# Optimization experiments

Hardware: AMD Instinct MI355X
Metric: run time of the kernel (lower is better)

## Reference

```python
import jax, jax.numpy as jnp
import numpy as np
import math

ANCHOR_SIZES = (128.0, 256.0, 512.0)
ANCHOR_RATIOS = (0.5, 1.0, 2.0)
NMS_THRESH = 0.7
PRE_NMS_TOPK = 6000   # rpn_test_prenms_topk (module is in eval at __init__)
POST_NMS_TOPK = 300   # rpn_test_topk
MIN_SIZE = 16.0
BBOX_CLIP = math.log(1000.0 / 16.0)


def _base_anchors():
    scales = jnp.array(ANCHOR_SIZES, jnp.float32)
    ratios = jnp.array(ANCHOR_RATIOS, jnp.float32)
    h_r = jnp.sqrt(ratios)
    w_r = 1.0 / h_r
    ws = (w_r[:, None] * scales[None, :]).reshape(-1)  # [A], ratio-major
    hs = (h_r[:, None] * scales[None, :]).reshape(-1)
    return jnp.stack([-ws, -hs, ws, hs], axis=1) * 0.5  # [A,4] centered at origin


def _grid_anchors(img_hw, feat_hw):
    Hi, Wi = img_hw
    Hf, Wf = feat_hw
    sy, sx = Hi // Hf, Wi // Wf  # feature stride
    shift_x = jnp.arange(Wf, dtype=jnp.float32) * sx
    shift_y = jnp.arange(Hf, dtype=jnp.float32) * sy
    yy, xx = jnp.meshgrid(shift_y, shift_x, indexing='ij')
    shifts = jnp.stack([xx, yy, xx, yy], axis=-1).reshape(-1, 1, 4)
    # layout (H, W, A) matches permute(0,2,3,1) flattening of the heads
    return (shifts + _base_anchors()[None]).reshape(-1, 4)


def _conv(x, w, b, pad):
    y = jax.lax.conv_general_dilated(x, w, (1, 1), pad,
                                     dimension_numbers=('NCHW', 'OIHW', 'NCHW'))
    return y + b[None, :, None, None]


def _decode(deltas, anchors):
    wa = anchors[:, 2] - anchors[:, 0]
    ha = anchors[:, 3] - anchors[:, 1]
    cxa = anchors[:, 0] + 0.5 * wa
    cya = anchors[:, 1] + 0.5 * ha
    dx, dy = deltas[:, 0], deltas[:, 1]
    dw = jnp.minimum(deltas[:, 2], BBOX_CLIP)
    dh = jnp.minimum(deltas[:, 3], BBOX_CLIP)
    cx = dx * wa + cxa
    cy = dy * ha + cya
    w = jnp.exp(dw) * wa
    h = jnp.exp(dh) * ha
    return jnp.stack([cx - 0.5 * w, cy - 0.5 * h, cx + 0.5 * w, cy + 0.5 * h], axis=1)


def _pairwise_iou(a, b):
    area_a = (a[:, 2] - a[:, 0]) * (a[:, 3] - a[:, 1])
    area_b = (b[:, 2] - b[:, 0]) * (b[:, 3] - b[:, 1])
    lt = jnp.maximum(a[:, None, :2], b[None, :, :2])
    rb = jnp.minimum(a[:, None, 2:], b[None, :, 2:])
    wh = jnp.clip(rb - lt, 0.0)
    inter = wh[..., 0] * wh[..., 1]
    return inter / (area_a[:, None] + area_b[None, :] - inter)


def _nms_keep(boxes, valid, thresh):
    # boxes are already sorted by descending score; greedy suppression
    N = boxes.shape[0]
    iou = _pairwise_iou(boxes, boxes)  # [N,N]
    idx = jnp.arange(N)

    def body(i, keep):
        sup = keep[i] & (iou[i] > thresh) & (idx > i)
        return keep & jnp.logical_not(sup)

    return jax.lax.fori_loop(0, N, body, valid)


def setup_inputs() -> dict:
    key = jax.random.key(0)
    ks = jax.random.split(key, 6)
    C, Hf, Wf = 1024, 100, 100
    Hi, Wi = 1600, 1600
    A = len(ANCHOR_SIZES) * len(ANCHOR_RATIOS)  # 9
    std = 0.01  # matches torch.nn.init.normal_(std=0.01), bias=0
    return {
        'input_image': jax.random.normal(ks[0], (1, 3, Hi, Wi), jnp.float32),
        'feature_map': jax.random.normal(ks[1], (1, C, Hf, Wf), jnp.float32),
        'conv_w': jax.random.normal(ks[2], (C, C, 3, 3), jnp.float32) * std,
        'conv_b': jnp.zeros((C,), jnp.float32),
        'obj_w': jax.random.normal(ks[3], (A, C, 1, 1), jnp.float32) * std,
        'obj_b': jnp.zeros((A,), jnp.float32),
        'reg_w': jax.random.normal(ks[4], (4 * A, C, 1, 1), jnp.float32) * std,
        'reg_b': jnp.zeros((4 * A,), jnp.float32),
    }


def reference(input_image, feature_map, conv_w, conv_b, obj_w, obj_b, reg_w, reg_b):
    Hi, Wi = input_image.shape[-2:]
    Hf, Wf = feature_map.shape[-2:]
    A = obj_w.shape[0]

    feats = jax.nn.relu(_conv(feature_map, conv_w, conv_b, 'SAME'))
    obj = _conv(feats, obj_w, obj_b, 'VALID')   # [N,A,Hf,Wf]
    reg = _conv(feats, reg_w, reg_b, 'VALID')   # [N,4A,Hf,Wf]

    obj_flat = jnp.transpose(obj, (0, 2, 3, 1)).reshape(-1)                 # [N*Hf*Wf*A]
    reg_flat = jnp.transpose(reg.reshape(-1, A, 4, Hf, Wf),
                             (0, 3, 4, 1, 2)).reshape(-1, 4)                # [N*Hf*Wf*A,4]

    anchors = _grid_anchors((Hi, Wi), (Hf, Wf))
    boxes = _decode(jax.lax.stop_gradient(reg_flat), anchors)
    probs = jax.nn.sigmoid(jax.lax.stop_gradient(obj_flat))

    k = min(PRE_NMS_TOPK, probs.shape[0])
    top_p, top_i = jax.lax.top_k(probs, k)
    b = boxes[top_i]
    b = jnp.stack([jnp.clip(b[:, 0], 0.0, Wi), jnp.clip(b[:, 1], 0.0, Hi),
                   jnp.clip(b[:, 2], 0.0, Wi), jnp.clip(b[:, 3], 0.0, Hi)], axis=1)
    valid = ((b[:, 2] - b[:, 0]) >= MIN_SIZE) & ((b[:, 3] - b[:, 1]) >= MIN_SIZE)

    keep = _nms_keep(b, valid, NMS_THRESH)
    masked = jnp.where(keep, top_p, -1.0)
    final_s, fi = jax.lax.top_k(masked, POST_NMS_TOPK)
    final_b = b[fi]
    good = final_s > 0.0  # zero-pad slots beyond the NMS survivor count
    proposals = jnp.where(good[:, None], final_b, 0.0)
    scores = jnp.where(good, final_s, 0.0)
    return proposals, scores
```

## Files before the change

kernel.cpp:

```cpp
#include <hip/hip_runtime.h>
#include <stdint.h>

typedef unsigned int uint32;
typedef unsigned long long uint64;

#define NPIX      10000
#define NCH       1024
#define NANCH     90000
#define PRE_TOPK  6000
#define POST_TOPK 300
#define SORT_N    8192
#define NWORDS    94
#define SUP_ROWS  6016
#define BBOX_CLIP_F 4.135166556742356f

#define TILE_H   8
#define TILE_W   16
#define HALO_H   10
#define HALO_W   18
#define HALO_WP  20
#define CICHUNK  16
#define C_PER_WAVE 16

__device__ __forceinline__ uint64 shfl64(uint64 v, int lane) {
    int lo = __shfl((int)(uint32)v, lane);
    int hi = __shfl((int)(uint32)(v >> 32), lane);
    return ((uint64)(uint32)hi << 32) | (uint32)lo;
}

__global__ __launch_bounds__(256) void zero_out(float* __restrict__ out, int n) {
    int i = blockIdx.x * 256 + threadIdx.x;
    if (i < n) out[i] = 0.f;
}

__global__ __launch_bounds__(256) void repack_w3(const float* __restrict__ w, float* __restrict__ W3) {
    int cot = blockIdx.x;
    int cib = blockIdx.y;
    int t = threadIdx.x;
    int c = t & 15;
    int cil = t >> 4;
    int ci = (cib << 6) | (cil << 2);
    int co = (cot << 4) | c;
#pragma unroll
    for (int r = 0; r < 4; ++r) {
        const float* src = w + ((size_t)co * 1024 + (ci + r)) * 9;
        float* dst = W3 + (((size_t)cot * 1024 + (ci + r)) * 9) * 16 + c;
#pragma unroll
        for (int kk = 0; kk < 9; ++kk)
            dst[kk * 16] = src[kk];
    }
}

__global__ __launch_bounds__(256) void conv_sw2(const float* __restrict__ fm,
        const float* __restrict__ W3, const float* __restrict__ bias,
        float* __restrict__ feats) {
    __shared__ float xt[CICHUNK][HALO_H][HALO_WP];
    const int t = threadIdx.x;
    const int lane = t & 63;
    const int wv = t >> 6;
    const int tile = blockIdx.x;
    const int tx0 = (tile % 7) * TILE_W;
    const int ty0 = (tile / 7) * TILE_H;
    const int cot = __builtin_amdgcn_readfirstlane((blockIdx.y << 2) + wv);
    const int co0 = cot << 4;
    const int ly = lane >> 3, lx = lane & 7;

    float acc0[C_PER_WAVE] = {};
    float acc1[C_PER_WAVE] = {};

#pragma unroll 1
    for (int c0 = 0; c0 < NCH; c0 += CICHUNK) {
        __syncthreads();
        for (int i = t; i < CICHUNK * HALO_H * HALO_W; i += 256) {
            int ci = i / (HALO_H * HALO_W);
            int rem = i - ci * (HALO_H * HALO_W);
            int hy = rem / HALO_W;
            int hx = rem - hy * HALO_W;
            int gy = ty0 - 1 + hy;
            int gx = tx0 - 1 + hx;
            bool ok = (gy >= 0) & (gy < 100) & (gx >= 0) & (gx < 100);
            xt[ci][hy][hx] = ok ? fm[(size_t)(c0 + ci) * NPIX + gy * 100 + gx] : 0.f;
        }
        __syncthreads();
#pragma unroll 1
        for (int ci = 0; ci < CICHUNK; ++ci) {
            const float* wb = W3 + (((size_t)cot * 1024 + (size_t)(c0 + ci)) * 9) * 16;
#pragma unroll
            for (int kk = 0; kk < 9; ++kk) {
                const int ky = kk / 3, kx2 = kk % 3;
                float x0v = xt[ci][ly + ky][lx + kx2];
                float x1v = xt[ci][ly + ky][lx + 8 + kx2];
#pragma unroll
                for (int c = 0; c < C_PER_WAVE; ++c) {
                    float wgt = wb[kk * 16 + c];
                    acc0[c] = fmaf(wgt, x0v, acc0[c]);
                    acc1[c] = fmaf(wgt, x1v, acc1[c]);
                }
            }
        }
    }

    const int gy = ty0 + ly;
    const int gx0 = tx0 + lx;
    const int gx1 = tx0 + 8 + lx;
    const bool oky = gy < 100;
#pragma unroll
    for (int c = 0; c < C_PER_WAVE; ++c) {
        float b = bias[co0 + c];
        if (oky && (gx0 < 100)) feats[(size_t)(co0 + c) * NPIX + gy * 100 + gx0] = fmaxf(acc0[c] + b, 0.f);
        if (oky && (gx1 < 100)) feats[(size_t)(co0 + c) * NPIX + gy * 100 + gx1] = fmaxf(acc1[c] + b, 0.f);
    }
}

__global__ __launch_bounds__(256) void heads(const float* __restrict__ feats,
        const float* __restrict__ objw, const float* __restrict__ objb,
        const float* __restrict__ regw, const float* __restrict__ regb,
        uint32* __restrict__ keys32, float* __restrict__ regflat) {
    int p0 = blockIdx.x << 6;
    int t = threadIdx.x;
    int pl = t & 63;
    int g = t >> 6;
    __shared__ float fts[64][65];
    __shared__ float wl[48][64];
    float acc[12] = {};
    for (int c0 = 0; c0 < 1024; c0 += 64) {
        __syncthreads();
#pragma unroll
        for (int r = 0; r < 16; ++r) {
            int cc = g + (r << 2);
            int p = p0 + pl;
            fts[cc][pl] = (p < NPIX) ? feats[(size_t)(c0 + cc) * NPIX + p] : 0.f;
        }
#pragma unroll
        for (int i = 0; i < 12; ++i) {
            int flat = (i << 8) + t;
            int o = flat >> 6;
            int cc = flat & 63;
            float v = 0.f;
            if (o < 9) v = objw[o * 1024 + c0 + cc];
            else if (o < 45) v = regw[(o - 9) * 1024 + c0 + cc];
            wl[o][cc] = v;
        }
        __syncthreads();
#pragma unroll 16
        for (int cc = 0; cc < 64; ++cc) {
            float v = fts[cc][pl];
#pragma unroll
            for (int i = 0; i < 12; ++i)
                acc[i] = fmaf(v, wl[g + (i << 2)][cc], acc[i]);
        }
    }
    int p = p0 + pl;
    if (p < NPIX) {
#pragma unroll
        for (int i = 0; i < 12; ++i) {
            int o = g + (i << 2);
            if (o < 9) {
                float logit = acc[i] + objb[o];
                float prob = 1.f / (1.f + expf(-logit));
                keys32[p * 9 + o] = 0xFFFFFFFFu - __float_as_uint(prob);
            } else if (o < 45) {
                int ch = o - 9;
                float v = acc[i] + regb[ch];
                int a = ch >> 2, d = ch & 3;
                regflat[((size_t)p * 9 + a) * 4 + d] = v;
            }
        }
    }
}

__global__ __launch_bounds__(1024) void radix_select(const uint32* __restrict__ keys, uint32* __restrict__ meta) {
    __shared__ uint32 hist[256];
    __shared__ uint32 sPrefix, sK;
    int t = threadIdx.x;
    if (t == 0) { sPrefix = 0; sK = PRE_TOPK; }
    for (int pass = 0; pass < 4; ++pass) {
        int shift = 24 - pass * 8;
        uint32 kmask = pass ? (0xFFFFFFFFu << (32 - 8 * pass)) : 0u;
        if (t < 256) hist[t] = 0;
        __syncthreads();
        uint32 pref = sPrefix;
        for (int i = t; i < NANCH; i += 1024) {
            uint32 k = keys[i];
            if ((k & kmask) == pref) atomicAdd(&hist[(k >> shift) & 255], 1u);
        }
        __syncthreads();
        if (t == 0) {
            uint32 cum = 0, K = sK;
            for (int b = 0; b < 256; ++b) {
                uint32 c = hist[b];
                if (cum + c >= K) { sPrefix = pref | ((uint32)b << shift); sK = K - cum; break; }
                cum += c;
            }
        }
        __syncthreads();
    }
    if (t == 0) meta[0] = sPrefix;
}

__global__ __launch_bounds__(256) void compact_k(const uint32* __restrict__ keys, const uint32* __restrict__ meta,
        uint32* __restrict__ cnt, uint64* __restrict__ sel) {
    int i = blockIdx.x * 256 + threadIdx.x;
    if (i >= NANCH) return;
    uint32 T = meta[0];
    uint32 k = keys[i];
    if (k <= T) {
        uint32 pos = atomicAdd(cnt, 1u);
        if (pos < SORT_N) sel[pos] = ((uint64)k << 32) | (uint32)i;
    }
}

__global__ __launch_bounds__(1024) void bitonic_sort(const uint32* __restrict__ meta, const uint64* __restrict__ sel,
        uint64* __restrict__ sorted) {
    __shared__ uint64 arr[SORT_N];
    int t = threadIdx.x;
    uint32 cnt = meta[1]; if (cnt > SORT_N) cnt = SORT_N;
    for (int i = t; i < SORT_N; i += 1024) arr[i] = (i < (int)cnt) ? sel[i] : 0xFFFFFFFFFFFFFFFFull;
    __syncthreads();
    for (unsigned k = 2; k <= SORT_N; k <<= 1) {
        for (unsigned j = k >> 1; j > 0; j >>= 1) {
#pragma unroll 1
            for (int s = 0; s < SORT_N / 1024; ++s) {
                unsigned i = s * 1024 + t;
                unsigned l = i ^ j;
                if (l > i) {
                    uint64 a = arr[i], b = arr[l];
                    bool up = ((i & k) == 0);
                    if ((a > b) == up) { arr[i] = b; arr[l] = a; }
                }
            }
            __syncthreads();
        }
    }
    for (int i = t; i < PRE_TOPK; i += 1024) sorted[i] = arr[i];
}

__global__ __launch_bounds__(256) void decode_k(const uint64* __restrict__ sorted,
        const float* __restrict__ regflat,
        float4* __restrict__ boxes, float* __restrict__ probv, uint32* __restrict__ valid) {
    int i = blockIdx.x * 256 + threadIdx.x;
    if (i >= PRE_TOPK) return;
    uint64 v = sorted[i];
    uint32 idx = (uint32)v;
    uint32 key = (uint32)(v >> 32);
    float prob = __uint_as_float(0xFFFFFFFFu - key);
    int a = idx % 9;
    int p = idx / 9;
    int y = p / 100;
    int x = p - y * 100;
    const float ratios[3] = {0.5f, 1.0f, 2.0f};
    const float scales[3] = {128.f, 256.f, 512.f};
    float ratio = ratios[a / 3];
    float scale = scales[a % 3];
    float h_r = sqrtf(ratio);
    float w_r = 1.0f / h_r;
    float wsz = w_r * scale;
    float hsz = h_r * scale;
    float sx = 16.f * (float)x;
    float sy = 16.f * (float)y;
    float ax1 = sx - wsz * 0.5f;
    float ay1 = sy - hsz * 0.5f;
    float ax2 = sx + wsz * 0.5f;
    float ay2 = sy + hsz * 0.5f;
    float wa = ax2 - ax1;
    float ha = ay2 - ay1;
    float cxa = ax1 + 0.5f * wa;
    float cya = ay1 + 0.5f * ha;
    float dx = regflat[(size_t)idx * 4 + 0];
    float dy = regflat[(size_t)idx * 4 + 1];
    float dw = fminf(regflat[(size_t)idx * 4 + 2], BBOX_CLIP_F);
    float dh = fminf(regflat[(size_t)idx * 4 + 3], BBOX_CLIP_F);
    float cx = dx * wa + cxa;
    float cy = dy * ha + cya;
    float w = expf(dw) * wa;
    float h = expf(dh) * ha;
    float x1 = cx - 0.5f * w, y1 = cy - 0.5f * h, x2 = cx + 0.5f * w, y2 = cy + 0.5f * h;
    x1 = fminf(fmaxf(x1, 0.f), 1600.f);
    y1 = fminf(fmaxf(y1, 0.f), 1600.f);
    x2 = fminf(fmaxf(x2, 0.f), 1600.f);
    y2 = fminf(fmaxf(y2, 0.f), 1600.f);
    boxes[i] = make_float4(x1, y1, x2, y2);
    probv[i] = prob;
    valid[i] = (((x2 - x1) >= 16.f) & ((y2 - y1) >= 16.f)) ? 1u : 0u;
}

__global__ __launch_bounds__(64) void nms_pairs(const float4* __restrict__ boxes, uint64* __restrict__ sup) {
    int bi = blockIdx.y, bj = blockIdx.x;
    int t = threadIdx.x;
    int i = bi * 64 + t;
    if (bj < bi) { if (i < SUP_ROWS) sup[(size_t)i * NWORDS + bj] = 0; return; }
    __shared__ float4 bx[64];
    __shared__ float ab[64];
    int j0 = bj * 64;
    float4 bb = (j0 + t < PRE_TOPK) ? boxes[j0 + t] : make_float4(0, 0, 0, 0);
    bx[t] = bb;
    ab[t] = (bb.z - bb.x) * (bb.w - bb.y);
    __syncthreads();
    uint64 bits = 0;
    if (i < PRE_TOPK) {
        float4 ba = boxes[i];
        float aa = (ba.z - ba.x) * (ba.w - ba.y);
        for (int jj = 0; jj < 64; ++jj) {
            int j = j0 + jj;
            if (j > i && j < PRE_TOPK) {
                float4 bv = bx[jj];
                float ltx = fmaxf(ba.x, bv.x);
                float lty = fmaxf(ba.y, bv.y);
                float rbx = fminf(ba.z, bv.z);
                float rby = fminf(ba.w, bv.w);
                float wv = fmaxf(rbx - ltx, 0.f);
                float hv = fmaxf(rby - lty, 0.f);
                float inter = wv * hv;
                float iou = inter / (aa + ab[jj] - inter);
                if (iou > 0.7f) bits |= (1ull << jj);
            }
        }
    }
    if (i < SUP_ROWS) sup[(size_t)i * NWORDS + bj] = bits;
}

__global__ __launch_bounds__(64) void nms_scan(const uint32* __restrict__ valid, const uint64* __restrict__ sup,
        uint32* __restrict__ keeplist, uint32* __restrict__ kcount) {
    int l = threadIdx.x;
    __shared__ uint64 srow[64][95];
    uint64 r0 = 0, r1 = 0;
    for (int b = 0; b < 64; ++b) {
        int idx = l * 64 + b;
        if (idx < PRE_TOPK && valid[idx]) r0 |= (1ull << b);
    }
    if (l < NWORDS - 64) {
        int base = (64 + l) * 64;
        for (int b = 0; b < 64; ++b) {
            int idx = base + b;
            if (idx < PRE_TOPK && valid[idx]) r1 |= (1ull << b);
        }
    }
    int outc = 0;
    bool done = false;
    for (int c = 0; c < NWORDS && !done; ++c) {
        __syncthreads();
        for (int rr = 0; rr < 64; ++rr) {
            int row = c * 64 + rr;
            srow[rr][l] = sup[(size_t)row * NWORDS + l];
            if (l < NWORDS - 64) srow[rr][64 + l] = sup[(size_t)row * NWORDS + 64 + l];
        }
        __syncthreads();
        for (int ii = 0; ii < 64; ++ii) {
            int i = c * 64 + ii;
            if (i >= PRE_TOPK) break;
            uint64 kw = (c < 64) ? shfl64(r0, c) : shfl64(r1, c - 64);
            if ((kw >> ii) & 1ull) {
                if (l == 0) keeplist[outc] = (uint32)i;
                ++outc;
                if (outc >= POST_TOPK) { done = true; break; }
                r0 &= ~srow[ii][l];
                if (l < NWORDS - 64) r1 &= ~srow[ii][64 + l];
            }
        }
    }
    if (l == 0) *kcount = (uint32)outc;
}

__global__ __launch_bounds__(512) void finalize_k(const uint32* __restrict__ keeplist, const uint32* __restrict__ kcount,
        const float4* __restrict__ boxes, const float* __restrict__ probv, float* __restrict__ out) {
    int t = threadIdx.x;
    if (t < POST_TOPK) {
        uint32 kc = *kcount;
        if (t < (int)kc) {
            int i = keeplist[t];
            float4 b = boxes[i];
            out[t * 4 + 0] = b.x; out[t * 4 + 1] = b.y; out[t * 4 + 2] = b.z; out[t * 4 + 3] = b.w;
            out[1200 + t] = probv[i];
        } else {
            out[t * 4 + 0] = 0.f; out[t * 4 + 1] = 0.f; out[t * 4 + 2] = 0.f; out[t * 4 + 3] = 0.f;
            out[1200 + t] = 0.f;
        }
    }
}

extern "C" void kernel_launch(void* const* d_in, const int* in_sizes, int n_in,
                              void* d_out, int out_size, void* d_ws, size_t ws_size,
                              hipStream_t stream) {
    const float* fm = (const float*)d_in[1];
    const float* cw = (const float*)d_in[2];
    const float* cb = (const float*)d_in[3];
    const float* ow = (const float*)d_in[4];
    const float* ob = (const float*)d_in[5];
    const float* rw = (const float*)d_in[6];
    const float* rb = (const float*)d_in[7];
    float* out = (float*)d_out;

    uint8_t* base = (uint8_t*)d_ws;
    size_t off = 0;
    auto alloc = [&](size_t bytes) -> void* {
        void* p = base + off;
        off = (off + bytes + 255) & ~(size_t)255;
        return p;
    };
    float* feats    = (float*)alloc((size_t)NCH * NPIX * 4);
    uint32* meta    = (uint32*)alloc(64);
    uint32* keepl   = (uint32*)alloc(POST_TOPK * 4);
    uint32* kcount  = (uint32*)alloc(64);
    size_t ubase = off;
    float* W3       = (float*)alloc((size_t)64 * 1024 * 9 * 16 * 4);
    size_t endA = off;
    off = ubase;
    uint32* keys    = (uint32*)alloc((size_t)NANCH * 4);
    float* regflat  = (float*)alloc((size_t)NANCH * 4 * 4);
    uint64* sel     = (uint64*)alloc((size_t)SORT_N * 8);
    uint64* sorted  = (uint64*)alloc((size_t)PRE_TOPK * 8);
    float4* boxes   = (float4*)alloc((size_t)PRE_TOPK * 16);
    float* probv    = (float*)alloc((size_t)PRE_TOPK * 4);
    uint32* validb  = (uint32*)alloc((size_t)PRE_TOPK * 4);
    uint64* sup     = (uint64*)alloc((size_t)SUP_ROWS * NWORDS * 8);
    size_t endB = off;
    size_t needed = (endA > endB) ? endA : endB;

    if (needed > ws_size) {
        zero_out<<<(out_size + 255) / 256, 256, 0, stream>>>(out, out_size);
        return;
    }

    hipMemsetAsync(meta, 0, 64, stream);

    repack_w3<<<dim3(64, 16), 256, 0, stream>>>(cw, W3);
    conv_sw2<<<dim3(91, 16), 256, 0, stream>>>(fm, W3, cb, feats);
    heads<<<157, 256, 0, stream>>>(feats, ow, ob, rw, rb, keys, regflat);
    radix_select<<<1, 1024, 0, stream>>>(keys, meta);
    compact_k<<<(NANCH + 255) / 256, 256, 0, stream>>>(keys, meta, meta + 1, sel);
    bitonic_sort<<<1, 1024, 0, stream>>>(meta, sel, sorted);
    decode_k<<<(PRE_TOPK + 255) / 256, 256, 0, stream>>>(sorted, regflat, boxes, probv, validb);
    nms_pairs<<<dim3(NWORDS, NWORDS), 64, 0, stream>>>(boxes, sup);
    nms_scan<<<1, 64, 0, stream>>>(validb, sup, keepl, kcount);
    finalize_k<<<1, 512, 0, stream>>>(keepl, kcount, boxes, probv, out);
}
```

Baseline: 3.361 ms.

## Double-buffer conv input halo and register-block adjacent output pixels

The 3x3 conv kernel now double-buffers its shared-memory input halo, loading the next channel chunk while computing the current one, so only one barrier is needed per chunk. Each lane now owns two horizontally adjacent output pixels and loads a 3x4 register window once per input channel with float2 LDS reads, instead of doing 18 scalar LDS reads. Staging uses a fixed thread-to-element mapping without integer division, and outputs are written as float2. The cost is double the LDS footprint, and the staging loads are issued synchronously into the other buffer, so latency hiding relies on the compiler scheduling them.

```diff
diff --git a/kernel.cpp b/kernel.cpp
--- a/kernel.cpp
+++ b/kernel.cpp
@@ -51,10 +51,10 @@
     }
 }
 
-__global__ __launch_bounds__(256) void conv_sw2(const float* __restrict__ fm,
+__global__ __launch_bounds__(256) void conv_v3(const float* __restrict__ fm,
         const float* __restrict__ W3, const float* __restrict__ bias,
         float* __restrict__ feats) {
-    __shared__ float xt[CICHUNK][HALO_H][HALO_WP];
+    __shared__ float xt[2][CICHUNK][HALO_H][HALO_WP];
     const int t = threadIdx.x;
     const int lane = t & 63;
     const int wv = t >> 6;
@@ -63,52 +63,74 @@
     const int ty0 = (tile / 7) * TILE_H;
     const int cot = __builtin_amdgcn_readfirstlane((blockIdx.y << 2) + wv);
     const int co0 = cot << 4;
-    const int ly = lane >> 3, lx = lane & 7;
+    const int ly = lane >> 3;
+    const int lxp = lane & 7;
+
+    const int sci = t >> 4;
+    const int sc = t & 15;
 
     float acc0[C_PER_WAVE] = {};
     float acc1[C_PER_WAVE] = {};
 
+    auto stage = [&](int buf, int c0) {
+        const float* src = fm + (size_t)(c0 + sci) * NPIX;
+#pragma unroll
+        for (int hy = 0; hy < HALO_H; ++hy) {
+            int gy = ty0 - 1 + hy;
+            int gx = tx0 - 1 + sc;
+            bool okr = (gy >= 0) & (gy < 100);
+            bool ok = okr & (gx >= 0) & (gx < 100);
+            xt[buf][sci][hy][sc] = ok ? src[gy * 100 + gx] : 0.f;
+            if (sc < HALO_W - 16) {
+                int gx2 = gx + 16;
+                bool ok2 = okr & (gx2 < 100);
+                xt[buf][sci][hy][sc + 16] = ok2 ? src[gy * 100 + gx2] : 0.f;
+            }
+        }
+    };
+
+    stage(0, 0);
+    __syncthreads();
+
 #pragma unroll 1
-    for (int c0 = 0; c0 < NCH; c0 += CICHUNK) {
-        __syncthreads();
-        for (int i = t; i < CICHUNK * HALO_H * HALO_W; i += 256) {
-            int ci = i / (HALO_H * HALO_W);
-            int rem = i - ci * (HALO_H * HALO_W);
-            int hy = rem / HALO_W;
-            int hx = rem - hy * HALO_W;
-            int gy = ty0 - 1 + hy;
-            int gx = tx0 - 1 + hx;
-            bool ok = (gy >= 0) & (gy < 100) & (gx >= 0) & (gx < 100);
-            xt[ci][hy][hx] = ok ? fm[(size_t)(c0 + ci) * NPIX + gy * 100 + gx] : 0.f;
-        }
-        __syncthreads();
+    for (int cc = 0; cc < NCH / CICHUNK; ++cc) {
+        const int cur = cc & 1;
+        if (cc + 1 < NCH / CICHUNK) stage(cur ^ 1, (cc + 1) * CICHUNK);
 #pragma unroll 1
         for (int ci = 0; ci < CICHUNK; ++ci) {
-            const float* wb = W3 + (((size_t)cot * 1024 + (size_t)(c0 + ci)) * 9) * 16;
+            const float* wb = W3 + (((size_t)cot * 1024 + (size_t)(cc * CICHUNK + ci)) * 9) * 16;
+            float w[3][4];
+#pragma unroll
+            for (int r = 0; r < 3; ++r) {
+                float2 lo = *(const float2*)&xt[cur][ci][ly + r][2 * lxp];
+                float2 hi = *(const float2*)&xt[cur][ci][ly + r][2 * lxp + 2];
+                w[r][0] = lo.x; w[r][1] = lo.y; w[r][2] = hi.x; w[r][3] = hi.y;
+            }
 #pragma unroll
             for (int kk = 0; kk < 9; ++kk) {
-                const int ky = kk / 3, kx2 = kk % 3;
-                float x0v = xt[ci][ly + ky][lx + kx2];
-                float x1v = xt[ci][ly + ky][lx + 8 + kx2];
+                const int ky = kk / 3, kx = kk % 3;
+                float x0 = w[ky][kx];
+                float x1 = w[ky][kx + 1];
 #pragma unroll
                 for (int c = 0; c < C_PER_WAVE; ++c) {
                     float wgt = wb[kk * 16 + c];
-                    acc0[c] = fmaf(wgt, x0v, acc0[c]);
-                    acc1[c] = fmaf(wgt, x1v, acc1[c]);
+                    acc0[c] = fmaf(wgt, x0, acc0[c]);
+                    acc1[c] = fmaf(wgt, x1, acc1[c]);
                 }
             }
         }
+        __syncthreads();
     }
 
     const int gy = ty0 + ly;
-    const int gx0 = tx0 + lx;
-    const int gx1 = tx0 + 8 + lx;
-    const bool oky = gy < 100;
-#pragma unroll
-    for (int c = 0; c < C_PER_WAVE; ++c) {
-        float b = bias[co0 + c];
-        if (oky && (gx0 < 100)) feats[(size_t)(co0 + c) * NPIX + gy * 100 + gx0] = fmaxf(acc0[c] + b, 0.f);
-        if (oky && (gx1 < 100)) feats[(size_t)(co0 + c) * NPIX + gy * 100 + gx1] = fmaxf(acc1[c] + b, 0.f);
+    const int gx0 = tx0 + 2 * lxp;
+    if ((gy < 100) & (gx0 < 100)) {
+#pragma unroll
+        for (int c = 0; c < C_PER_WAVE; ++c) {
+            float b = bias[co0 + c];
+            float2 v = make_float2(fmaxf(acc0[c] + b, 0.f), fmaxf(acc1[c] + b, 0.f));
+            *(float2*)&feats[(size_t)(co0 + c) * NPIX + gy * 100 + gx0] = v;
+        }
     }
 }
 
@@ -424,7 +446,7 @@
     hipMemsetAsync(meta, 0, 64, stream);
 
     repack_w3<<<dim3(64, 16), 256, 0, stream>>>(cw, W3);
-    conv_sw2<<<dim3(91, 16), 256, 0, stream>>>(fm, W3, cb, feats);
+    conv_v3<<<dim3(91, 16), 256, 0, stream>>>(fm, W3, cb, feats);
     heads<<<157, 256, 0, stream>>>(feats, ow, ob, rw, rb, keys, regflat);
     radix_select<<<1, 1024, 0, stream>>>(keys, meta);
     compact_k<<<(NANCH + 255) / 256, 256, 0, stream>>>(keys, meta, meta + 1, sel);
```

Result: slower. 3.781 ms (+12.5%).
